# Kernel optimization log

Measured on AMD Instinct MI355X. Metric: run time of the kernel, lower is better.

Reference implementation:

```python
import jax, jax.numpy as jnp
import numpy as np

DIM = 256
HEADS = 8
DHEAD = 64
MEM = 4
HID = HEADS * DHEAD  # 512


def setup_inputs() -> dict:
    key = jax.random.key(0)
    k1, k2, k3, k4 = jax.random.split(key, 4)
    x = jax.random.normal(k1, (2, DIM, 48, 48), jnp.float32)
    gamma = jnp.zeros((DIM, 1, 1), jnp.float32)  # nn.Parameter init is zeros
    mem_kv = jax.random.normal(k2, (2, HEADS, MEM, DHEAD), jnp.float32)
    w_qkv = jax.random.normal(k3, (3 * HID, DIM), jnp.float32) * 0.05  # 1x1 conv weight
    w_out = jax.random.normal(k4, (DIM, HID), jnp.float32) * 0.05     # 1x1 conv weight
    return {"x": x, "gamma": gamma, "mem_kv": mem_kv, "w_qkv": w_qkv, "w_out": w_out}


def reference(x, gamma, mem_kv, w_qkv, w_out):
    b, c, h, w = x.shape
    scale = DHEAD ** -0.5
    # RMSNorm: F.normalize along channel dim (L2, eps=1e-12) * (gamma+1) * sqrt(dim)
    l2 = jnp.sqrt(jnp.sum(x * x, axis=1, keepdims=True))
    xn = x / jnp.maximum(l2, 1e-12) * (gamma + 1.0) * (c ** 0.5)
    # 1x1 conv to qkv: [b, 3*HID, h, w]
    qkv = jnp.einsum('oc,bchw->bohw', w_qkv, xn)
    qkv = qkv.reshape(b, 3, HEADS, DHEAD, h * w)
    # (b, heads, n, dhead)
    q = jnp.swapaxes(qkv[:, 0], 2, 3)
    k = jnp.swapaxes(qkv[:, 1], 2, 3)
    v = jnp.swapaxes(qkv[:, 2], 2, 3)
    # prepend learnable memory kv tokens
    mk = jnp.broadcast_to(mem_kv[0], (b, HEADS, MEM, DHEAD))
    mv = jnp.broadcast_to(mem_kv[1], (b, HEADS, MEM, DHEAD))
    k = jnp.concatenate([mk, k], axis=2)
    v = jnp.concatenate([mv, v], axis=2)
    sim = jnp.einsum('bhid,bhjd->bhij', q * scale, k)
    attn = jax.nn.softmax(sim, axis=-1)
    out = jnp.einsum('bhij,bhjd->bhid', attn, v)
    out = jnp.swapaxes(out, 2, 3).reshape(b, HID, h, w)
    return jnp.einsum('oc,bchw->bohw', w_out, out)
```

## Files before the change

kernel.cpp:

```cpp
#include <hip/hip_runtime.h>

#define BATCH 2
#define CDIM 256
#define NPIX 2304
#define NHEAD 8
#define DH 64
#define HID 512
#define NMEM 4
#define NKV 2308
#define NKVP 2368
#define QSCALE 0.125f
#define LOG2E 1.4426950408889634f
#define WQKV_E 393216
#define WOUT_E 131072
#define KVSPLIT 1216

typedef float f32x4 __attribute__((ext_vector_type(4)));
typedef __bf16 bf16x8 __attribute__((ext_vector_type(8)));
typedef unsigned short u16;
typedef u16 u16x4 __attribute__((ext_vector_type(4)));
typedef u16 u16x8 __attribute__((ext_vector_type(8)));
typedef unsigned u32x2 __attribute__((ext_vector_type(2)));

#if __has_builtin(__builtin_amdgcn_exp2f)
#define EXP2(x) __builtin_amdgcn_exp2f(x)
#else
#define EXP2(x) exp2f(x)
#endif

static __device__ __forceinline__ u16 f2b(float f) {
  union { float f; unsigned u; } a; a.f = f;
  unsigned u = a.u;
  u += 0x7fffu + ((u >> 16) & 1u);
  return (u16)(u >> 16);
}
static __device__ __forceinline__ float b2f(u16 b) {
  union { float f; unsigned u; } a; a.u = ((unsigned)b) << 16; return a.f;
}

__global__ __launch_bounds__(256) void k_prep(
    const float* __restrict__ wqkv, const float* __restrict__ wout,
    const float* __restrict__ gamma, const float* __restrict__ mem_kv,
    const float* __restrict__ x,
    u16* __restrict__ wb, u16* __restrict__ kk, u16* __restrict__ vT,
    u16* __restrict__ xnT)
{
  __shared__ float xs[16 * 261];
  __shared__ float red[16][17];
  __shared__ float rsh[16];
  const int blk = blockIdx.x, t = threadIdx.x;
  if (blk < 256) {
    const int i0 = (blk * 256 + t) * 8;
    u16x8 o;
    if (i0 < WQKV_E) {
      const float sc = ((i0 >> 8) < 512) ? QSCALE * LOG2E : 1.0f;
      const int c0 = i0 & 255;
      const f32x4 a = *(const f32x4*)&wqkv[i0];
      const f32x4 b = *(const f32x4*)&wqkv[i0 + 4];
      const f32x4 g0 = *(const f32x4*)&gamma[c0];
      const f32x4 g1 = *(const f32x4*)&gamma[c0 + 4];
#pragma unroll
      for (int e = 0; e < 4; ++e) {
        o[e]     = f2b(a[e] * sc * (1.0f + g0[e]));
        o[e + 4] = f2b(b[e] * sc * (1.0f + g1[e]));
      }
    } else {
      const f32x4 a = *(const f32x4*)&wout[i0 - WQKV_E];
      const f32x4 b = *(const f32x4*)&wout[i0 - WQKV_E + 4];
#pragma unroll
      for (int e = 0; e < 4; ++e) { o[e] = f2b(a[e]); o[e + 4] = f2b(b[e]); }
    }
    *(u16x8*)&wb[i0] = o;
  } else if (blk < 272) {
    const int idx = (blk - 256) * 256 + t;
    const int d = idx & 63;
    const int m = (idx >> 6) & 3;
    const int h = (idx >> 8) & 7;
    const int b = idx >> 11;
    const float mk = mem_kv[((size_t)h * NMEM + m) * DH + d];
    const float mv = mem_kv[(((size_t)NHEAD + h) * NMEM + m) * DH + d];
    kk[(((size_t)(b * NHEAD + h)) * NKV + m) * DH + d] = f2b(mk);
    vT[(((size_t)(b * NHEAD + h)) * DH + d) * NKVP + m] = f2b(mv);
  } else if (blk < 336) {
    const int gid = (blk - 272) * 256 + t;
    const int row = gid >> 4;
    const int c0 = (gid & 15) * 4 + 2304;
    u16x4 z = {0, 0, 0, 0};
    *(u16x4*)&vT[(size_t)row * NKVP + c0] = z;
  } else {
    const int blk2 = blk - 336;
    const int b = blk2 / 144;
    const int p0 = (blk2 % 144) * 16;
    const int px = t & 15, cg = t >> 4;
    const float* xb = x + (size_t)b * CDIM * NPIX + p0 + px;
    float ssq = 0.f;
#pragma unroll
    for (int i = 0; i < 16; ++i) {
      const int c = cg * 16 + i;
      const float v = xb[(size_t)c * NPIX];
      xs[px * 261 + c] = v;
      ssq += v * v;
    }
    red[px][cg] = ssq;
    __syncthreads();
    if (t < 16) {
      float s = 0.f;
#pragma unroll
      for (int i = 0; i < 16; ++i) s += red[t][i];
      rsh[t] = 16.0f / fmaxf(sqrtf(s), 1e-12f);
    }
    __syncthreads();
    {
      const int pp = t >> 4, c0 = (t & 15) * 16;
      const float rs = rsh[pp];
      u16x8 o0, o1;
#pragma unroll
      for (int e = 0; e < 8; ++e) {
        o0[e] = f2b(xs[pp * 261 + c0 + e] * rs);
        o1[e] = f2b(xs[pp * 261 + c0 + 8 + e] * rs);
      }
      u16* dst = &xnT[(size_t)(b * NPIX + p0 + pp) * CDIM + c0];
      *(u16x8*)dst = o0;
      *(u16x8*)(dst + 8) = o1;
    }
  }
}

__global__ __launch_bounds__(512) void k_qkv(
    const u16* __restrict__ xnT, const u16* __restrict__ wb,
    u16* __restrict__ q, u16* __restrict__ kk, u16* __restrict__ vT)
{
  __shared__ __align__(16) u16 bs[128 * 256];
  const int t = threadIdx.x, w = t >> 6, l = t & 63, li = l & 15, kg = l >> 4;
  const int m0 = blockIdx.x * 128 + w * 16;
  const int n0 = blockIdx.y * 128;
  {
    const int brow = t >> 2, bcs = (t & 3) * 64;
    const int bsw = (brow & 7) * 8;
    const u16* wsrc = wb + (size_t)(n0 + brow) * CDIM + bcs;
#pragma unroll
    for (int j = 0; j < 8; ++j) {
      const u16x8 v = *(const u16x8*)&wsrc[j * 8];
      *(u16x8*)&bs[brow * 256 + ((bcs + j * 8) ^ bsw)] = v;
    }
  }
  const u16* ap = xnT + (size_t)(m0 + li) * CDIM + kg * 8;
  const int lsw = (li & 7) * 8;
  f32x4 acc[8];
#pragma unroll
  for (int cf = 0; cf < 8; ++cf) { f32x4 z = {0.f,0.f,0.f,0.f}; acc[cf] = z; }
  __syncthreads();
#pragma unroll
  for (int ks = 0; ks < 8; ++ks) {
    const bf16x8 af = *(const bf16x8*)(ap + ks * 32);
#pragma unroll
    for (int cf = 0; cf < 8; ++cf) {
      const int row = cf * 16 + li;
      const bf16x8 bfr = *(const bf16x8*)&bs[row * 256 + ((ks * 32 + kg * 8) ^ lsw)];
      acc[cf] = __builtin_amdgcn_mfma_f32_16x16x32_bf16(af, bfr, acc[cf], 0, 0, 0);
    }
  }
  const int bb = (m0 >= NPIX) ? 1 : 0;
  const int plbase = m0 - bb * NPIX + kg * 4;
#pragma unroll
  for (int cf = 0; cf < 8; ++cf) {
    const int o0f = n0 + cf * 16;
    const int r = o0f >> 9, oo = o0f & 511, h = oo >> 6, d = (oo & 63) + li;
    if (r == 0) {
      u16* base = q + ((size_t)(bb * NHEAD + h) * NPIX + plbase) * DH + d;
#pragma unroll
      for (int rr = 0; rr < 4; ++rr) base[(size_t)rr * DH] = f2b(acc[cf][rr]);
    } else if (r == 1) {
      u16* base = kk + ((size_t)(bb * NHEAD + h) * NKV + NMEM + plbase) * DH + d;
#pragma unroll
      for (int rr = 0; rr < 4; ++rr) base[(size_t)rr * DH] = f2b(acc[cf][rr]);
    } else {
      u16x4 pk;
#pragma unroll
      for (int rr = 0; rr < 4; ++rr) pk[rr] = f2b(acc[cf][rr]);
      *(u16x4*)&vT[(((size_t)(bb * NHEAD + h)) * DH + d) * NKVP + NMEM + plbase] = pk;
    }
  }
}

__global__ __launch_bounds__(512) void k_attn(
    const u16* __restrict__ q, const u16* __restrict__ kk, const u16* __restrict__ vT,
    u16* __restrict__ aoB)
{
  __shared__ __align__(16) char smem[51200];
  u16* kbuf = (u16*)smem;
  u16* vbuf = (u16*)(smem + 16384);
  u16* ps   = (u16*)(smem + 32768);
  float* accbuf = (float*)smem;
  float* mlbuf  = (float*)(smem + 17152);
  const int t = threadIdx.x;
  const int w = t >> 6, l = t & 63;
  const int qsub = w & 3, hf = w >> 2;
  const int li = l & 15, kg = l >> 4;
  const int id = blockIdx.x;
  const int xcd = id & 7, slot = id >> 3;
  const int yl = (slot >= 36) ? 1 : 0;
  const int xq = slot - yl * 36;
  const int bh = xcd * 2 + yl;
  const int b = bh >> 3, hh = bh & 7;
  const int qrow0 = xq * 64 + qsub * 16;
  const u16* qp = q + ((size_t)bh * NPIX + qrow0) * DH;
  const u16* kp = kk + (size_t)bh * NKV * DH;
  const u16* vp = vT + (size_t)bh * DH * NKVP;

  const bf16x8 bq0 = *(const bf16x8*)&qp[li * DH + kg * 8];
  const bf16x8 bq1 = *(const bf16x8*)&qp[li * DH + 32 + kg * 8];

  const int hft = t >> 8;
  const int tt = t & 255;
  const int srow = tt >> 3;
  const int scol = (tt & 7) * 8;
  const int ssw = (srow & 7) * 8;
  const int sbase = hft * KVSPLIT;
  u16* kdst0 = &kbuf[hft * 4096 + srow * 64 + (scol ^ ssw)];
  u16* kdst1 = &kbuf[hft * 4096 + (srow + 32) * 64 + (scol ^ ssw)];
  u16* vdst0 = &vbuf[hft * 4096 + srow * 64 + (scol ^ ssw)];
  u16* vdst1 = &vbuf[hft * 4096 + (srow + 32) * 64 + (scol ^ ssw)];

  f32x4 acc[4];
#pragma unroll
  for (int df = 0; df < 4; ++df) { f32x4 z = {0.f,0.f,0.f,0.f}; acc[df] = z; }
  float m = -1e30f, lsum = 0.f;
  const int cbase0 = hf * KVSPLIT;

  u16x8 rk0, rk1, rv0, rv1;
  rk0 = *(const u16x8*)&kp[(size_t)(sbase + srow) * DH + scol];
  rk1 = *(const u16x8*)&kp[(size_t)(sbase + srow + 32) * DH + scol];
  rv0 = *(const u16x8*)&vp[(size_t)srow * NKVP + sbase + scol];
  rv1 = *(const u16x8*)&vp[(size_t)(srow + 32) * NKVP + sbase + scol];

  const int NT = 19;
#pragma unroll 1
  for (int i = 0; i < NT; ++i) {
    __syncthreads();
    *(u16x8*)kdst0 = rk0;
    *(u16x8*)kdst1 = rk1;
    *(u16x8*)vdst0 = rv0;
    *(u16x8*)vdst1 = rv1;
    if (i + 1 < NT) {
      int nb = sbase + (i + 1) * 64;
      int snb = (nb > NKVP - 64) ? (NKVP - 64) : nb;
      int kr0 = nb + srow;      if (kr0 > NKV - 1) kr0 = NKV - 1;
      int kr1 = nb + srow + 32; if (kr1 > NKV - 1) kr1 = NKV - 1;
      rk0 = *(const u16x8*)&kp[(size_t)kr0 * DH + scol];
      rk1 = *(const u16x8*)&kp[(size_t)kr1 * DH + scol];
      rv0 = *(const u16x8*)&vp[(size_t)srow * NKVP + snb + scol];
      rv1 = *(const u16x8*)&vp[(size_t)(srow + 32) * NKVP + snb + scol];
    }
    __syncthreads();
    const int kbase = cbase0 + i * 64;
    if (kbase < NKV) {
      const bool lastt = (kbase + 64 > NKV);
      const u16* kb = &kbuf[hf * 4096];
      const u16* vb = &vbuf[hf * 4096];
      f32x4 s[4];
#pragma unroll
      for (int jf = 0; jf < 4; ++jf) {
        const int row = jf * 16 + li;
        const int rsw = (row & 7) * 8;
        const bf16x8 ak0 = *(const bf16x8*)&kb[row * 64 + ((kg * 8) ^ rsw)];
        const bf16x8 ak1 = *(const bf16x8*)&kb[row * 64 + ((32 + kg * 8) ^ rsw)];
        f32x4 sf = {0.f, 0.f, 0.f, 0.f};
        sf = __builtin_amdgcn_mfma_f32_16x16x32_bf16(ak0, bq0, sf, 0, 0, 0);
        sf = __builtin_amdgcn_mfma_f32_16x16x32_bf16(ak1, bq1, sf, 0, 0, 0);
        s[jf] = sf;
      }
      if (lastt) {
#pragma unroll
        for (int jf = 0; jf < 4; ++jf)
#pragma unroll
          for (int r = 0; r < 4; ++r)
            if (kbase + jf * 16 + kg * 4 + r >= NKV) s[jf][r] = -1e30f;
      }
      float pmax = fmaxf(fmaxf(fmaxf(s[0][0], s[0][1]), fmaxf(s[0][2], s[0][3])),
                         fmaxf(fmaxf(s[1][0], s[1][1]), fmaxf(s[1][2], s[1][3])));
      pmax = fmaxf(pmax, fmaxf(fmaxf(fmaxf(s[2][0], s[2][1]), fmaxf(s[2][2], s[2][3])),
                               fmaxf(fmaxf(s[3][0], s[3][1]), fmaxf(s[3][2], s[3][3]))));
      pmax = fmaxf(pmax, __shfl_xor(pmax, 16));
      pmax = fmaxf(pmax, __shfl_xor(pmax, 32));
      if (__any(pmax > m + 8.0f)) {
        const float mn = fmaxf(m, pmax);
        const float al = EXP2(m - mn);
        m = mn;
        lsum *= al;
        float a4[4];
#pragma unroll
        for (int r = 0; r < 4; ++r) a4[r] = __shfl(al, (l & 48) | (kg * 4 + r));
#pragma unroll
        for (int df = 0; df < 4; ++df)
#pragma unroll
          for (int r = 0; r < 4; ++r) acc[df][r] *= a4[r];
      }
#pragma unroll
      for (int jf = 0; jf < 4; ++jf) {
        u32x2 wp;
#pragma unroll
        for (int rp = 0; rp < 2; ++rp) {
          const float e0 = EXP2(s[jf][rp * 2 + 0] - m);
          const float e1 = EXP2(s[jf][rp * 2 + 1] - m);
          lsum += e0 + e1;
          unsigned pk;
          asm("v_cvt_pk_bf16_f32 %0, %1, %2" : "=v"(pk) : "v"(e0), "v"(e1));
          wp[rp] = pk;
        }
        *(u32x2*)&ps[w * 1152 + li * 72 + jf * 16 + kg * 4] = wp;
      }
      asm volatile("s_waitcnt lgkmcnt(0)" ::: "memory");
      __builtin_amdgcn_sched_barrier(0);
      const bf16x8 ap0 = *(const bf16x8*)&ps[w * 1152 + li * 72 + kg * 8];
      const bf16x8 ap1 = *(const bf16x8*)&ps[w * 1152 + li * 72 + 32 + kg * 8];
#pragma unroll
      for (int df = 0; df < 4; ++df) {
        const int row = df * 16 + li;
        const int rsw = (row & 7) * 8;
        const bf16x8 bv0 = *(const bf16x8*)&vb[row * 64 + ((kg * 8) ^ rsw)];
        const bf16x8 bv1 = *(const bf16x8*)&vb[row * 64 + ((32 + kg * 8) ^ rsw)];
        acc[df] = __builtin_amdgcn_mfma_f32_16x16x32_bf16(ap0, bv0, acc[df], 0, 0, 0);
        acc[df] = __builtin_amdgcn_mfma_f32_16x16x32_bf16(ap1, bv1, acc[df], 0, 0, 0);
      }
    }
  }
  lsum += __shfl_xor(lsum, 16);
  lsum += __shfl_xor(lsum, 32);
  float m4[4], l4[4];
#pragma unroll
  for (int r = 0; r < 4; ++r) {
    const int src = (l & 48) | (kg * 4 + r);
    m4[r] = __shfl(m, src);
    l4[r] = __shfl(lsum, src);
  }
  __syncthreads();
  if (hf == 1) {
#pragma unroll
    for (int df = 0; df < 4; ++df)
#pragma unroll
      for (int r = 0; r < 4; ++r)
        accbuf[(qsub * 16 + kg * 4 + r) * 67 + df * 16 + li] = acc[df][r];
    if (kg == 0) {
      mlbuf[(qsub * 16 + li) * 2 + 0] = m;
      mlbuf[(qsub * 16 + li) * 2 + 1] = lsum;
    }
  }
  __syncthreads();
  if (hf == 0) {
    float f0[4], f1[4], rL[4];
#pragma unroll
    for (int r = 0; r < 4; ++r) {
      const float m1 = mlbuf[(qsub * 16 + kg * 4 + r) * 2 + 0];
      const float l1 = mlbuf[(qsub * 16 + kg * 4 + r) * 2 + 1];
      const float M = fmaxf(m4[r], m1);
      f0[r] = EXP2(m4[r] - M);
      f1[r] = EXP2(m1 - M);
      rL[r] = __builtin_amdgcn_rcpf(l4[r] * f0[r] + l1 * f1[r]);
    }
#pragma unroll
    for (int df = 0; df < 4; ++df)
#pragma unroll
      for (int r = 0; r < 4; ++r) {
        const float a1 = accbuf[(qsub * 16 + kg * 4 + r) * 67 + df * 16 + li];
        const float o = (acc[df][r] * f0[r] + a1 * f1[r]) * rL[r];
        aoB[((size_t)b * NPIX + qrow0 + kg * 4 + r) * HID + hh * DH + df * 16 + li] = f2b(o);
      }
  }
}

__global__ __launch_bounds__(256) void k_outg(
    const u16* __restrict__ aoB, const u16* __restrict__ wob, float* __restrict__ out)
{
  __shared__ __align__(16) u16 bs[64 * 512];
  const int t = threadIdx.x, w = t >> 6, l = t & 63, li = l & 15, kg = l >> 4;
  const int m0 = blockIdx.x * 64 + w * 16;
  const int n0 = blockIdx.y * 64;
  {
    const int brow = t >> 2, bcs = (t & 3) * 128;
    const int bsw = (brow & 7) * 8;
    const u16* wsrc = wob + (size_t)(n0 + brow) * HID + bcs;
#pragma unroll
    for (int j = 0; j < 16; ++j) {
      const u16x8 v = *(const u16x8*)&wsrc[j * 8];
      *(u16x8*)&bs[brow * 512 + ((bcs + j * 8) ^ bsw)] = v;
    }
  }
  const u16* ap = aoB + (size_t)(m0 + li) * HID + kg * 8;
  const int lsw = (li & 7) * 8;
  f32x4 acc[4];
#pragma unroll
  for (int cf = 0; cf < 4; ++cf) { f32x4 z = {0.f,0.f,0.f,0.f}; acc[cf] = z; }
  __syncthreads();
#pragma unroll
  for (int ks = 0; ks < 16; ++ks) {
    const bf16x8 af = *(const bf16x8*)(ap + ks * 32);
#pragma unroll
    for (int cf = 0; cf < 4; ++cf) {
      const int row = cf * 16 + li;
      const bf16x8 bf = *(const bf16x8*)&bs[row * 512 + ((ks * 32 + kg * 8) ^ lsw)];
      acc[cf] = __builtin_amdgcn_mfma_f32_16x16x32_bf16(af, bf, acc[cf], 0, 0, 0);
    }
  }
  const int bb = (m0 >= NPIX) ? 1 : 0;
  const int pl = m0 - bb * NPIX + kg * 4;
#pragma unroll
  for (int cf = 0; cf < 4; ++cf) {
    const int o = n0 + cf * 16 + li;
    *(f32x4*)&out[((size_t)(bb * CDIM + o)) * NPIX + pl] = acc[cf];
  }
}

extern "C" void kernel_launch(void* const* d_in, const int* in_sizes, int n_in,
                              void* d_out, int out_size, void* d_ws, size_t ws_size,
                              hipStream_t stream)
{
  const float* x      = (const float*)d_in[0];
  const float* gamma  = (const float*)d_in[1];
  const float* mem_kv = (const float*)d_in[2];
  const float* wqkv   = (const float*)d_in[3];
  const float* wout   = (const float*)d_in[4];
  float* out = (float*)d_out;
  char* ws = (char*)d_ws;
  const size_t XNT = (size_t)BATCH * NPIX * CDIM * sizeof(u16);
  const size_t WB  = (size_t)(WQKV_E + WOUT_E) * sizeof(u16);
  const size_t QB  = (size_t)BATCH * NHEAD * NPIX * DH * sizeof(u16);
  const size_t KB  = (size_t)BATCH * NHEAD * NKV  * DH * sizeof(u16);
  const size_t VTB = (size_t)BATCH * NHEAD * DH * NKVP * sizeof(u16);
  u16* xnT = (u16*)ws;
  u16* wb  = (u16*)(ws + XNT);
  u16* q   = (u16*)(ws + XNT + WB);
  u16* kk  = (u16*)(ws + XNT + WB + QB);
  u16* vT  = (u16*)(ws + XNT + WB + QB + KB);
  u16* aoB = (u16*)(ws + XNT + WB + QB + KB + VTB);

  k_prep<<<dim3(624), dim3(256), 0, stream>>>(wqkv, wout, gamma, mem_kv, x,
                                              wb, kk, vT, xnT);
  k_qkv<<<dim3(36, 12), dim3(512), 0, stream>>>(xnT, wb, q, kk, vT);
  k_attn<<<dim3(576), dim3(512), 0, stream>>>(q, kk, vT, aoB);
  k_outg<<<dim3(72, 4), dim3(256), 0, stream>>>(aoB, wb + WQKV_E, out);
}
```

Baseline: 87.74 us.

## Shrink attention blocks to 48 query rows with 6 waves and 768 blocks

The attention kernel now launches 768 blocks of 384 threads, each covering 48 query rows (3 waves per KV half) instead of 64 rows with 8 waves. This gives finer-grained blocks for better CU balance and uses less shared memory. The K/V staging is remapped so only 256 threads load, each fetching four 16-byte chunks per matrix. Cost: every block reloads the full K/V stream, so total K/V traffic rises, and the loader work now falls on fewer threads.

```diff
diff --git a/kernel.cpp b/kernel.cpp
--- a/kernel.cpp
+++ b/kernel.cpp
@@ -183,11 +183,11 @@
   }
 }
 
-__global__ __launch_bounds__(512) void k_attn(
+__global__ __launch_bounds__(384) void k_attn(
     const u16* __restrict__ q, const u16* __restrict__ kk, const u16* __restrict__ vT,
     u16* __restrict__ aoB)
 {
-  __shared__ __align__(16) char smem[51200];
+  __shared__ __align__(16) char smem[46592];
   u16* kbuf = (u16*)smem;
   u16* vbuf = (u16*)(smem + 16384);
   u16* ps   = (u16*)(smem + 32768);
@@ -195,15 +195,16 @@
   float* mlbuf  = (float*)(smem + 17152);
   const int t = threadIdx.x;
   const int w = t >> 6, l = t & 63;
-  const int qsub = w & 3, hf = w >> 2;
+  const int hf = (w >= 3) ? 1 : 0;
+  const int qsub = w - hf * 3;
   const int li = l & 15, kg = l >> 4;
   const int id = blockIdx.x;
   const int xcd = id & 7, slot = id >> 3;
-  const int yl = (slot >= 36) ? 1 : 0;
-  const int xq = slot - yl * 36;
+  const int yl = (slot >= 48) ? 1 : 0;
+  const int xq = slot - yl * 48;
   const int bh = xcd * 2 + yl;
   const int b = bh >> 3, hh = bh & 7;
-  const int qrow0 = xq * 64 + qsub * 16;
+  const int qrow0 = xq * 48 + qsub * 16;
   const u16* qp = q + ((size_t)bh * NPIX + qrow0) * DH;
   const u16* kp = kk + (size_t)bh * NKV * DH;
   const u16* vp = vT + (size_t)bh * DH * NKVP;
@@ -211,16 +212,14 @@
   const bf16x8 bq0 = *(const bf16x8*)&qp[li * DH + kg * 8];
   const bf16x8 bq1 = *(const bf16x8*)&qp[li * DH + 32 + kg * 8];
 
-  const int hft = t >> 8;
-  const int tt = t & 255;
-  const int srow = tt >> 3;
-  const int scol = (tt & 7) * 8;
+  const int hft = (t >> 7) & 1;
+  const int tt = t & 127;
+  const int srow = tt >> 1;
+  const int sc = (tt & 1) * 32;
   const int ssw = (srow & 7) * 8;
   const int sbase = hft * KVSPLIT;
-  u16* kdst0 = &kbuf[hft * 4096 + srow * 64 + (scol ^ ssw)];
-  u16* kdst1 = &kbuf[hft * 4096 + (srow + 32) * 64 + (scol ^ ssw)];
-  u16* vdst0 = &vbuf[hft * 4096 + srow * 64 + (scol ^ ssw)];
-  u16* vdst1 = &vbuf[hft * 4096 + (srow + 32) * 64 + (scol ^ ssw)];
+  u16* kdst = &kbuf[hft * 4096 + srow * 64];
+  u16* vdst = &vbuf[hft * 4096 + srow * 64];
 
   f32x4 acc[4];
 #pragma unroll
@@ -228,29 +227,36 @@
   float m = -1e30f, lsum = 0.f;
   const int cbase0 = hf * KVSPLIT;
 
-  u16x8 rk0, rk1, rv0, rv1;
-  rk0 = *(const u16x8*)&kp[(size_t)(sbase + srow) * DH + scol];
-  rk1 = *(const u16x8*)&kp[(size_t)(sbase + srow + 32) * DH + scol];
-  rv0 = *(const u16x8*)&vp[(size_t)srow * NKVP + sbase + scol];
-  rv1 = *(const u16x8*)&vp[(size_t)(srow + 32) * NKVP + sbase + scol];
+  u16x8 rk[4], rv[4];
+  if (t < 256) {
+    int kr = sbase + srow; if (kr > NKV - 1) kr = NKV - 1;
+#pragma unroll
+    for (int j = 0; j < 4; ++j) {
+      rk[j] = *(const u16x8*)&kp[(size_t)kr * DH + sc + j * 8];
+      rv[j] = *(const u16x8*)&vp[(size_t)srow * NKVP + sbase + sc + j * 8];
+    }
+  }
 
   const int NT = 19;
 #pragma unroll 1
   for (int i = 0; i < NT; ++i) {
     __syncthreads();
-    *(u16x8*)kdst0 = rk0;
-    *(u16x8*)kdst1 = rk1;
-    *(u16x8*)vdst0 = rv0;
-    *(u16x8*)vdst1 = rv1;
-    if (i + 1 < NT) {
-      int nb = sbase + (i + 1) * 64;
-      int snb = (nb > NKVP - 64) ? (NKVP - 64) : nb;
-      int kr0 = nb + srow;      if (kr0 > NKV - 1) kr0 = NKV - 1;
-      int kr1 = nb + srow + 32; if (kr1 > NKV - 1) kr1 = NKV - 1;
-      rk0 = *(const u16x8*)&kp[(size_t)kr0 * DH + scol];
-      rk1 = *(const u16x8*)&kp[(size_t)kr1 * DH + scol];
-      rv0 = *(const u16x8*)&vp[(size_t)srow * NKVP + snb + scol];
-      rv1 = *(const u16x8*)&vp[(size_t)(srow + 32) * NKVP + snb + scol];
+    if (t < 256) {
+#pragma unroll
+      for (int j = 0; j < 4; ++j) {
+        *(u16x8*)&kdst[(sc + j * 8) ^ ssw] = rk[j];
+        *(u16x8*)&vdst[(sc + j * 8) ^ ssw] = rv[j];
+      }
+      if (i + 1 < NT) {
+        const int nb = sbase + (i + 1) * 64;
+        const int snb = (nb > NKVP - 64) ? (NKVP - 64) : nb;
+        int kr = nb + srow; if (kr > NKV - 1) kr = NKV - 1;
+#pragma unroll
+        for (int j = 0; j < 4; ++j) {
+          rk[j] = *(const u16x8*)&kp[(size_t)kr * DH + sc + j * 8];
+          rv[j] = *(const u16x8*)&vp[(size_t)srow * NKVP + snb + sc + j * 8];
+        }
+      }
     }
     __syncthreads();
     const int kbase = cbase0 + i * 64;
@@ -437,6 +443,6 @@
   k_prep<<<dim3(624), dim3(256), 0, stream>>>(wqkv, wout, gamma, mem_kv, x,
                                               wb, kk, vT, xnT);
   k_qkv<<<dim3(36, 12), dim3(512), 0, stream>>>(xnT, wb, q, kk, vT);
-  k_attn<<<dim3(576), dim3(512), 0, stream>>>(q, kk, vT, aoB);
+  k_attn<<<dim3(768), dim3(384), 0, stream>>>(q, kk, vT, aoB);
   k_outg<<<dim3(72, 4), dim3(256), 0, stream>>>(aoB, wb + WQKV_E, out);
 }
```

Result: slower. 91.42 us (+4.2%).
